# Kernel tuning notes

Hardware: AMD Instinct MI355X
Metric: run time of the kernel (lower is better)

Reference implementation:

```python
import jax, jax.numpy as jnp
import numpy as np

H = 32  # hidden size per direction (hard-wired in module)


def _gru_scan(x_proj, W_hh, b_hh, reverse):
    """x_proj: [T, B, 3H] = x @ W_ih.T + b_ih (precomputed). Returns all hidden states [T, B, H].
    Gate order follows PyTorch: (r, z, n)."""
    def step(h, xp):
        gh = h @ W_hh.T + b_hh                      # [B, 3H]
        xr, xz, xn = jnp.split(xp, 3, axis=-1)
        hr, hz, hn = jnp.split(gh, 3, axis=-1)
        r = jax.nn.sigmoid(xr + hr)
        z = jax.nn.sigmoid(xz + hz)
        n = jnp.tanh(xn + r * hn)
        h_new = (1.0 - z) * n + z * h
        return h_new, h_new

    B = x_proj.shape[1]
    h0 = jnp.zeros((B, H), x_proj.dtype)
    _, ys = jax.lax.scan(step, h0, x_proj, reverse=reverse)
    return ys  # ys[t] = hidden after consuming x[t] (fwd) or x[T-1..t] (bwd)


def setup_inputs() -> dict:
    key = jax.random.key(0)
    ks = jax.random.split(key, 14)
    B, T = 2048, 512
    s_ih = 1.0 / np.sqrt(H)
    inp = {
        "x": jax.random.normal(ks[0], (B, T, 1), dtype=jnp.float32),
        # forward-direction GRU params (PyTorch layout: [3H, in], [3H, H], [3H])
        "W_ih_f": jax.random.uniform(ks[1], (3 * H, 1), jnp.float32, -s_ih, s_ih),
        "W_hh_f": jax.random.uniform(ks[2], (3 * H, H), jnp.float32, -s_ih, s_ih),
        "b_ih_f": jax.random.uniform(ks[3], (3 * H,), jnp.float32, -s_ih, s_ih),
        "b_hh_f": jax.random.uniform(ks[4], (3 * H,), jnp.float32, -s_ih, s_ih),
        # backward-direction GRU params
        "W_ih_b": jax.random.uniform(ks[5], (3 * H, 1), jnp.float32, -s_ih, s_ih),
        "W_hh_b": jax.random.uniform(ks[6], (3 * H, H), jnp.float32, -s_ih, s_ih),
        "b_ih_b": jax.random.uniform(ks[7], (3 * H,), jnp.float32, -s_ih, s_ih),
        "b_hh_b": jax.random.uniform(ks[8], (3 * H,), jnp.float32, -s_ih, s_ih),
        # MLP head: Linear(64,16) -> ReLU -> Linear(16,1) -> Sigmoid
        "W1": jax.random.uniform(ks[9], (16, 2 * H), jnp.float32, -0.125, 0.125),
        "b1": jax.random.uniform(ks[10], (16,), jnp.float32, -0.125, 0.125),
        "W2": jax.random.uniform(ks[11], (1, 16), jnp.float32, -0.25, 0.25),
        "b2": jax.random.uniform(ks[12], (1,), jnp.float32, -0.25, 0.25),
    }
    return inp


def reference(x, W_ih_f, W_hh_f, b_ih_f, b_hh_f,
              W_ih_b, W_hh_b, b_ih_b, b_hh_b,
              W1, b1, W2, b2):
    xt = jnp.swapaxes(x, 0, 1)                 # [T, B, 1]
    # Precompute input projections for all timesteps (input_size=1 so this is cheap)
    xpf = xt @ W_ih_f.T + b_ih_f               # [T, B, 3H]
    xpb = xt @ W_ih_b.T + b_ih_b               # [T, B, 3H]
    ys_f = _gru_scan(xpf, W_hh_f, b_hh_f, reverse=False)
    ys_b = _gru_scan(xpb, W_hh_b, b_hh_b, reverse=True)
    # out[:, -1, :] in torch = concat(fwd hidden at t=T-1, bwd hidden at t=T-1)
    out_last = jnp.concatenate([ys_f[-1], ys_b[-1]], axis=-1)   # [B, 64]
    h1 = jax.nn.relu(out_last @ W1.T + b1)                      # [B, 16]
    return jax.nn.sigmoid(h1 @ W2.T + b2)                       # [B, 1]
```

## Files before the change

kernel.cpp:

```cpp
#include <hip/hip_runtime.h>


typedef float vf4 __attribute__((ext_vector_type(4)));
typedef _Float16 f16;
typedef f16 h4 __attribute__((ext_vector_type(4)));
typedef f16 h8 __attribute__((ext_vector_type(8)));

#define TT 512
#define HH 32

#define LOG2E 1.44269504f

__device__ __forceinline__ float fast_sigm(float a) {
  return __builtin_amdgcn_rcpf(1.0f + __builtin_amdgcn_exp2f(-LOG2E * a));
}
__device__ __forceinline__ float fast_tanh(float a) {
  return __builtin_fmaf(-2.0f,
      __builtin_amdgcn_rcpf(1.0f + __builtin_amdgcn_exp2f(2.0f * LOG2E * a)),
      1.0f);
}

__global__ __launch_bounds__(256)
__attribute__((amdgpu_waves_per_eu(1, 1)))
void gru_bidir_head(const float* __restrict__ X,
                    const float* __restrict__ Wih_f, const float* __restrict__ Whh_f,
                    const float* __restrict__ bih_f, const float* __restrict__ bhh_f,
                    const float* __restrict__ Wih_b,
                    const float* __restrict__ bih_b, const float* __restrict__ bhh_b,
                    const float* __restrict__ W1, const float* __restrict__ b1,
                    const float* __restrict__ W2, const float* __restrict__ b2,
                    float* __restrict__ out)
{
  __shared__ float xbuf[8][TT];
  __shared__ f16   hbuf[4][2][HH];
  __shared__ float obuf[8][64];

  const int tid  = threadIdx.x;
  const int lane = tid & 63;
  const int wid  = tid >> 6;
  const int nh   = lane & 15;
  const int q    = lane >> 4;
  const int p    = q & 1;
  const int hsel = lane >> 5;
  const int j    = nh + 16 * hsel;
  const int rs   = 2 * wid + p;

  const int g32 = tid & 31, rsS = tid >> 5;
  const vf4* Xr4 = (const vf4*)(X + (size_t)((blockIdx.x << 3) + rsS) * TT);
  vf4* xb4 = (vf4*)&xbuf[rsS][0];
  #pragma unroll
  for (int qq = 0; qq < 4; ++qq) xb4[g32 + 32 * qq] = Xr4[g32 + 32 * qq];

  const float s1 = -LOG2E;
  const float s2 = 2.0f * LOG2E;

#define LDB(P, G, F, S) h8 P; { \
    const float* wr = Whh_f + (size_t)((G)*HH + nh + 16*(F)) * HH; \
    const int k1 = 4*q, k2 = 16 + 4*q; \
    P = (h8){ (f16)(wr[k1]*(S)), (f16)(wr[k1+1]*(S)), (f16)(wr[k1+2]*(S)), (f16)(wr[k1+3]*(S)), \
              (f16)(wr[k2]*(S)), (f16)(wr[k2+1]*(S)), (f16)(wr[k2+2]*(S)), (f16)(wr[k2+3]*(S)) }; }
  LDB(Br0, 0, 0, s1); LDB(Br1, 0, 1, s1);
  LDB(Bz0, 1, 0, s1); LDB(Bz1, 1, 1, s1);
  LDB(Bn0, 2, 0, s2); LDB(Bn1, 2, 1, s2);

  const float xwr = Wih_f[j] * s1, xwz = Wih_f[HH + j] * s1, xwn = Wih_f[2*HH + j] * s2;
  const float cbr = (bih_f[j]      + bhh_f[j])      * s1;
  const float cbz = (bih_f[HH + j] + bhh_f[HH + j]) * s1;
  const float cbn = bih_f[2*HH + j] * s2;
  const float cbh = bhh_f[2*HH + j] * s2;
  const vf4 Ch = { cbh, 0.0f, 0.0f, 0.0f };

  const int rowA = ((nh >> 2) + (nh & 3)) & 1;
  const h4* Alo = (const h4*)&hbuf[wid][rowA][4*q];
  const h4* Ahi = (const h4*)&hbuf[wid][rowA][16 + 4*q];
  f16* hwp = &hbuf[wid][p][j];

  float h = 0.0f;
  *hwp = (f16)0.0f;
  __builtin_amdgcn_wave_barrier();

  const vf4* xv = (const vf4*)&xbuf[rs][0];
  vf4 x4 = xv[0];

  #pragma unroll 1
  for (int tg = 0; tg < TT / 4; ++tg) {
    const vf4 x4n = xv[tg + 1 < TT / 4 ? tg + 1 : tg];

    const float sr0 = __builtin_fmaf(x4.x, xwr, cbr), sz0 = __builtin_fmaf(x4.x, xwz, cbz),
                sn0 = __builtin_fmaf(x4.x, xwn, cbn);
    const float sr1 = __builtin_fmaf(x4.y, xwr, cbr), sz1 = __builtin_fmaf(x4.y, xwz, cbz),
                sn1 = __builtin_fmaf(x4.y, xwn, cbn);
    const float sr2 = __builtin_fmaf(x4.z, xwr, cbr), sz2 = __builtin_fmaf(x4.z, xwz, cbz),
                sn2 = __builtin_fmaf(x4.z, xwn, cbn);
    const float sr3 = __builtin_fmaf(x4.w, xwr, cbr), sz3 = __builtin_fmaf(x4.w, xwz, cbz),
                sn3 = __builtin_fmaf(x4.w, xwn, cbn);

    #pragma unroll
    for (int u = 0; u < 4; ++u) {
      const float sr = (u == 0) ? sr0 : (u == 1) ? sr1 : (u == 2) ? sr2 : sr3;
      const float sz = (u == 0) ? sz0 : (u == 1) ? sz1 : (u == 2) ? sz2 : sz3;
      const float sn = (u == 0) ? sn0 : (u == 1) ? sn1 : (u == 2) ? sn2 : sn3;

      const h4 alo = *Alo, ahi = *Ahi;
      const h8 A = (h8){alo[0], alo[1], alo[2], alo[3],
                        ahi[0], ahi[1], ahi[2], ahi[3]};

      const vf4 Cr = { sr, 0.0f, 0.0f, 0.0f };
      const vf4 Cz = { sz, 0.0f, 0.0f, 0.0f };
      const vf4 Dr0 = __builtin_amdgcn_mfma_f32_16x16x32_f16(A, Br0, Cr, 0, 0, 0);
      const vf4 Dr1 = __builtin_amdgcn_mfma_f32_16x16x32_f16(A, Br1, Cr, 0, 0, 0);
      const vf4 Dz0 = __builtin_amdgcn_mfma_f32_16x16x32_f16(A, Bz0, Cz, 0, 0, 0);
      const vf4 Dz1 = __builtin_amdgcn_mfma_f32_16x16x32_f16(A, Bz1, Cz, 0, 0, 0);
      const vf4 Dn0 = __builtin_amdgcn_mfma_f32_16x16x32_f16(A, Bn0, Ch, 0, 0, 0);
      const vf4 Dn1 = __builtin_amdgcn_mfma_f32_16x16x32_f16(A, Bn1, Ch, 0, 0, 0);

      const float ar = hsel ? Dr1[0] : Dr0[0];
      const float az = hsel ? Dz1[0] : Dz0[0];
      const float an = hsel ? Dn1[0] : Dn0[0];

      const float r  = __builtin_amdgcn_rcpf(1.0f + __builtin_amdgcn_exp2f(ar));
      const float z  = __builtin_amdgcn_rcpf(1.0f + __builtin_amdgcn_exp2f(az));
      const float y  = __builtin_fmaf(r, an, sn);
      const float nn = __builtin_fmaf(-2.0f,
          __builtin_amdgcn_rcpf(1.0f + __builtin_amdgcn_exp2f(y)), 1.0f);
      h = __builtin_fmaf(z, h - nn, nn);

      *hwp = (f16)h;
      __builtin_amdgcn_wave_barrier();
    }
    x4 = x4n;
  }

  obuf[rs][j] = h;
  __syncthreads();

  const float xl  = xbuf[rsS][TT - 1];
  const float rbv = fast_sigm(__builtin_fmaf(xl, Wih_b[g32],      bih_b[g32]      + bhh_b[g32]));
  const float zbv = fast_sigm(__builtin_fmaf(xl, Wih_b[HH + g32], bih_b[HH + g32] + bhh_b[HH + g32]));
  const float xnb = __builtin_fmaf(xl, Wih_b[2*HH + g32], bih_b[2*HH + g32]);
  const float nbv = fast_tanh(__builtin_fmaf(rbv, bhh_b[2*HH + g32], xnb));
  const float hbv = nbv - zbv * nbv;

  obuf[rsS][32 + g32] = hbv;
  __builtin_amdgcn_wave_barrier();

  const int jj = g32 & 15;
  const vf4* W1r = (const vf4*)(W1 + jj * 64);
  const vf4* hc  = (const vf4*)&obuf[rsS][0];
  vf4 a4 = W1r[0] * hc[0];
  #pragma unroll
  for (int qq = 1; qq < 16; ++qq)
    a4 = __builtin_elementwise_fma(W1r[qq], hc[qq], a4);
  float acc = b1[jj] + (a4.x + a4.y) + (a4.z + a4.w);
  float h1v = fmaxf(acc, 0.0f) * W2[jj];
  h1v += __shfl_down(h1v, 8, 16);
  h1v += __shfl_down(h1v, 4, 16);
  h1v += __shfl_down(h1v, 2, 16);
  h1v += __shfl_down(h1v, 1, 16);
  if (g32 == 0) out[(blockIdx.x << 3) + rsS] = fast_sigm(h1v + b2[0]);
}

extern "C" void kernel_launch(void* const* d_in, const int* in_sizes, int n_in,
                              void* d_out, int out_size, void* d_ws, size_t ws_size,
                              hipStream_t stream) {
  const float* X     = (const float*)d_in[0];
  const float* Wih_f = (const float*)d_in[1];
  const float* Whh_f = (const float*)d_in[2];
  const float* bih_f = (const float*)d_in[3];
  const float* bhh_f = (const float*)d_in[4];
  const float* Wih_b = (const float*)d_in[5];
  const float* bih_b = (const float*)d_in[7];
  const float* bhh_b = (const float*)d_in[8];
  const float* W1    = (const float*)d_in[9];
  const float* b1    = (const float*)d_in[10];
  const float* W2    = (const float*)d_in[11];
  const float* b2    = (const float*)d_in[12];
  float* out = (float*)d_out;

  gru_bidir_head<<<256, 256, 0, stream>>>(X, Wih_f, Whh_f, bih_f, bhh_f,
                                          Wih_b, bih_b, bhh_b, W1, b1, W2, b2, out);
}
```

Baseline: 154.6 us.

## Exchange GRU hidden state via permlane swap and bpermute instead of LDS

Replaces the per-step LDS write/read of the f16 hidden state with register-level exchange: convert to f16, swap halves with v_permlane32_swap, pack pairs, and gather the MFMA A operand via four ds_bpermute calls. The B operand K-ordering is interleaved to match the new packed layout. The gate math is also reordered so z*h is computed off the critical tanh path. This aims to shorten the serial per-timestep latency chain, at the risk of bpermute latency being comparable to LDS and of layout mistakes.

```diff
diff --git a/kernel.cpp b/kernel.cpp
--- a/kernel.cpp
+++ b/kernel.cpp
@@ -2,8 +2,8 @@
 
 
 typedef float vf4 __attribute__((ext_vector_type(4)));
+typedef int   vi4 __attribute__((ext_vector_type(4)));
 typedef _Float16 f16;
-typedef f16 h4 __attribute__((ext_vector_type(4)));
 typedef f16 h8 __attribute__((ext_vector_type(8)));
 
 #define TT 512
@@ -32,7 +32,6 @@
                     float* __restrict__ out)
 {
   __shared__ float xbuf[8][TT];
-  __shared__ f16   hbuf[4][2][HH];
   __shared__ float obuf[8][64];
 
   const int tid  = threadIdx.x;
@@ -57,8 +56,10 @@
 #define LDB(P, G, F, S) h8 P; { \
     const float* wr = Whh_f + (size_t)((G)*HH + nh + 16*(F)) * HH; \
     const int k1 = 4*q, k2 = 16 + 4*q; \
-    P = (h8){ (f16)(wr[k1]*(S)), (f16)(wr[k1+1]*(S)), (f16)(wr[k1+2]*(S)), (f16)(wr[k1+3]*(S)), \
-              (f16)(wr[k2]*(S)), (f16)(wr[k2+1]*(S)), (f16)(wr[k2+2]*(S)), (f16)(wr[k2+3]*(S)) }; }
+    P = (h8){ (f16)(wr[k1  ]*(S)), (f16)(wr[k2  ]*(S)), \
+              (f16)(wr[k1+1]*(S)), (f16)(wr[k2+1]*(S)), \
+              (f16)(wr[k1+2]*(S)), (f16)(wr[k2+2]*(S)), \
+              (f16)(wr[k1+3]*(S)), (f16)(wr[k2+3]*(S)) }; }
   LDB(Br0, 0, 0, s1); LDB(Br1, 0, 1, s1);
   LDB(Bz0, 1, 0, s1); LDB(Bz1, 1, 1, s1);
   LDB(Bn0, 2, 0, s2); LDB(Bn1, 2, 1, s2);
@@ -70,15 +71,10 @@
   const float cbh = bhh_f[2*HH + j] * s2;
   const vf4 Ch = { cbh, 0.0f, 0.0f, 0.0f };
 
-  const int rowA = ((nh >> 2) + (nh & 3)) & 1;
-  const h4* Alo = (const h4*)&hbuf[wid][rowA][4*q];
-  const h4* Ahi = (const h4*)&hbuf[wid][rowA][16 + 4*q];
-  f16* hwp = &hbuf[wid][p][j];
+  const int lsrc4 = ((((lane >> 2) & 1) << 4) + ((lane >> 4) << 2)) << 2;
 
   float h = 0.0f;
-  *hwp = (f16)0.0f;
-  __builtin_amdgcn_wave_barrier();
-
+  h8 A = {};
   const vf4* xv = (const vf4*)&xbuf[rs][0];
   vf4 x4 = xv[0];
 
@@ -101,10 +97,6 @@
       const float sz = (u == 0) ? sz0 : (u == 1) ? sz1 : (u == 2) ? sz2 : sz3;
       const float sn = (u == 0) ? sn0 : (u == 1) ? sn1 : (u == 2) ? sn2 : sn3;
 
-      const h4 alo = *Alo, ahi = *Ahi;
-      const h8 A = (h8){alo[0], alo[1], alo[2], alo[3],
-                        ahi[0], ahi[1], ahi[2], ahi[3]};
-
       const vf4 Cr = { sr, 0.0f, 0.0f, 0.0f };
       const vf4 Cz = { sz, 0.0f, 0.0f, 0.0f };
       const vf4 Dr0 = __builtin_amdgcn_mfma_f32_16x16x32_f16(A, Br0, Cr, 0, 0, 0);
@@ -118,15 +110,28 @@
       const float az = hsel ? Dz1[0] : Dz0[0];
       const float an = hsel ? Dn1[0] : Dn0[0];
 
-      const float r  = __builtin_amdgcn_rcpf(1.0f + __builtin_amdgcn_exp2f(ar));
-      const float z  = __builtin_amdgcn_rcpf(1.0f + __builtin_amdgcn_exp2f(az));
-      const float y  = __builtin_fmaf(r, an, sn);
-      const float nn = __builtin_fmaf(-2.0f,
+      const float z   = __builtin_amdgcn_rcpf(1.0f + __builtin_amdgcn_exp2f(az));
+      const float zh  = z * h;
+      const float omz = 1.0f - z;
+      const float r   = __builtin_amdgcn_rcpf(1.0f + __builtin_amdgcn_exp2f(ar));
+      const float y   = __builtin_fmaf(r, an, sn);
+      const float nn  = __builtin_fmaf(-2.0f,
           __builtin_amdgcn_rcpf(1.0f + __builtin_amdgcn_exp2f(y)), 1.0f);
-      h = __builtin_fmaf(z, h - nn, nn);
+      h = __builtin_fmaf(omz, nn, zh);
 
-      *hwp = (f16)h;
-      __builtin_amdgcn_wave_barrier();
+      unsigned hf;
+      asm("v_cvt_f16_f32 %0, %1" : "=v"(hf) : "v"(h));
+      unsigned plo = hf, phi = hf;
+      asm volatile("v_permlane32_swap_b32 %0, %1" : "+v"(plo), "+v"(phi));
+      unsigned P;
+      asm("v_pack_b32_f16 %0, %1, %2" : "=v"(P) : "v"(plo), "v"(phi));
+      const int a0 = __builtin_amdgcn_ds_bpermute(lsrc4,      (int)P);
+      const int a1 = __builtin_amdgcn_ds_bpermute(lsrc4 + 4,  (int)P);
+      const int a2 = __builtin_amdgcn_ds_bpermute(lsrc4 + 8,  (int)P);
+      const int a3 = __builtin_amdgcn_ds_bpermute(lsrc4 + 12, (int)P);
+      union { vi4 i; h8 v; } ua;
+      ua.i = (vi4){a0, a1, a2, a3};
+      A = ua.v;
     }
     x4 = x4n;
   }
```

Result: slower. 159.8 us (+3.3%).

## Interleave hidden-state LDS layout, double-buffer h, and shorten gate dependency chain

Applied to the files above, without the earlier changes.

Stores the fp16 hidden state interleaved so each lane reads its eight A-operand values with a single 128-bit LDS load instead of two 64-bit loads plus a repack, and reorders the weight B fragments to match the new K order. Hidden state is now double-buffered across alternating timesteps. The GRU update is also rewritten so the z-dependent terms are computed while the r/tanh chain is still in flight, which shortens the serial critical path. The double buffer relies on wave_barrier ordering within a single wave, and the K permutation has to match exactly between the A and B operands.

```diff
diff --git a/kernel.cpp b/kernel.cpp
--- a/kernel.cpp
+++ b/kernel.cpp
@@ -3,7 +3,6 @@
 
 typedef float vf4 __attribute__((ext_vector_type(4)));
 typedef _Float16 f16;
-typedef f16 h4 __attribute__((ext_vector_type(4)));
 typedef f16 h8 __attribute__((ext_vector_type(8)));
 
 #define TT 512
@@ -31,9 +30,9 @@
                     const float* __restrict__ W2, const float* __restrict__ b2,
                     float* __restrict__ out)
 {
-  __shared__ float xbuf[8][TT];
-  __shared__ f16   hbuf[4][2][HH];
-  __shared__ float obuf[8][64];
+  __shared__ float    xbuf[8][TT];
+  __shared__ unsigned hp[2][4][2][16];
+  __shared__ float    obuf[8][64];
 
   const int tid  = threadIdx.x;
   const int lane = tid & 63;
@@ -57,8 +56,10 @@
 #define LDB(P, G, F, S) h8 P; { \
     const float* wr = Whh_f + (size_t)((G)*HH + nh + 16*(F)) * HH; \
     const int k1 = 4*q, k2 = 16 + 4*q; \
-    P = (h8){ (f16)(wr[k1]*(S)), (f16)(wr[k1+1]*(S)), (f16)(wr[k1+2]*(S)), (f16)(wr[k1+3]*(S)), \
-              (f16)(wr[k2]*(S)), (f16)(wr[k2+1]*(S)), (f16)(wr[k2+2]*(S)), (f16)(wr[k2+3]*(S)) }; }
+    P = (h8){ (f16)(wr[k1  ]*(S)), (f16)(wr[k2  ]*(S)), \
+              (f16)(wr[k1+1]*(S)), (f16)(wr[k2+1]*(S)), \
+              (f16)(wr[k1+2]*(S)), (f16)(wr[k2+2]*(S)), \
+              (f16)(wr[k1+3]*(S)), (f16)(wr[k2+3]*(S)) }; }
   LDB(Br0, 0, 0, s1); LDB(Br1, 0, 1, s1);
   LDB(Bz0, 1, 0, s1); LDB(Bz1, 1, 1, s1);
   LDB(Bn0, 2, 0, s2); LDB(Bn1, 2, 1, s2);
@@ -70,13 +71,14 @@
   const float cbh = bhh_f[2*HH + j] * s2;
   const vf4 Ch = { cbh, 0.0f, 0.0f, 0.0f };
 
-  const int rowA = ((nh >> 2) + (nh & 3)) & 1;
-  const h4* Alo = (const h4*)&hbuf[wid][rowA][4*q];
-  const h4* Ahi = (const h4*)&hbuf[wid][rowA][16 + 4*q];
-  f16* hwp = &hbuf[wid][p][j];
+  const int Rr = (lane >> 2) & 1;
+  const h8* rp0 = (const h8*)&hp[0][wid][Rr][q << 2];
+  const h8* rp1 = (const h8*)&hp[1][wid][Rr][q << 2];
+  unsigned short* wp0 = (unsigned short*)&hp[0][wid][p][nh] + hsel;
+  unsigned short* wp1 = (unsigned short*)&hp[1][wid][p][nh] + hsel;
 
   float h = 0.0f;
-  *hwp = (f16)0.0f;
+  *wp0 = 0; *wp1 = 0;
   __builtin_amdgcn_wave_barrier();
 
   const vf4* xv = (const vf4*)&xbuf[rs][0];
@@ -101,9 +103,7 @@
       const float sz = (u == 0) ? sz0 : (u == 1) ? sz1 : (u == 2) ? sz2 : sz3;
       const float sn = (u == 0) ? sn0 : (u == 1) ? sn1 : (u == 2) ? sn2 : sn3;
 
-      const h4 alo = *Alo, ahi = *Ahi;
-      const h8 A = (h8){alo[0], alo[1], alo[2], alo[3],
-                        ahi[0], ahi[1], ahi[2], ahi[3]};
+      const h8 A = (u & 1) ? *rp1 : *rp0;
 
       const vf4 Cr = { sr, 0.0f, 0.0f, 0.0f };
       const vf4 Cz = { sz, 0.0f, 0.0f, 0.0f };
@@ -118,14 +118,17 @@
       const float az = hsel ? Dz1[0] : Dz0[0];
       const float an = hsel ? Dn1[0] : Dn0[0];
 
-      const float r  = __builtin_amdgcn_rcpf(1.0f + __builtin_amdgcn_exp2f(ar));
-      const float z  = __builtin_amdgcn_rcpf(1.0f + __builtin_amdgcn_exp2f(az));
-      const float y  = __builtin_fmaf(r, an, sn);
-      const float nn = __builtin_fmaf(-2.0f,
-          __builtin_amdgcn_rcpf(1.0f + __builtin_amdgcn_exp2f(y)), 1.0f);
-      h = __builtin_fmaf(z, h - nn, nn);
+      const float z    = __builtin_amdgcn_rcpf(1.0f + __builtin_amdgcn_exp2f(az));
+      const float omz  = 1.0f - z;
+      const float base = __builtin_fmaf(z, h, omz);
+      const float m2   = __builtin_fmaf(2.0f, z, -2.0f);
+      const float r    = __builtin_amdgcn_rcpf(1.0f + __builtin_amdgcn_exp2f(ar));
+      const float y    = __builtin_fmaf(r, an, sn);
+      const float w    = __builtin_amdgcn_rcpf(1.0f + __builtin_amdgcn_exp2f(y));
+      h = __builtin_fmaf(m2, w, base);
 
-      *hwp = (f16)h;
+      union { f16 f; unsigned short u16; } cc; cc.f = (f16)h;
+      if (u & 1) *wp0 = cc.u16; else *wp1 = cc.u16;
       __builtin_amdgcn_wave_barrier();
     }
     x4 = x4n;
```

Result: faster. 150.9 us (-2.4%).
